# Optimization experiments

Measured on AMD Instinct MI355X. Metric: run time of the kernel, lower is better.

Reference implementation:

```python
import jax, jax.numpy as jnp
import numpy as np

D_MODEL = 1024
HEADS = 16
D_K = D_MODEL // HEADS
B, S = 2, 2048


def setup_inputs() -> dict:
    key = jax.random.key(0)
    ks = jax.random.split(key, 11)
    sc = 1.0 / np.sqrt(D_MODEL)
    return {
        "q": jax.random.normal(ks[0], (B, S, D_MODEL), jnp.float32),
        "k": jax.random.normal(ks[1], (B, S, D_MODEL), jnp.float32),
        "v": jax.random.normal(ks[2], (B, S, D_MODEL), jnp.float32),
        "Wq": jax.random.normal(ks[3], (D_MODEL, D_MODEL), jnp.float32) * sc,
        "bq": jnp.zeros((D_MODEL,), jnp.float32),
        "Wk": jax.random.normal(ks[4], (D_MODEL, D_MODEL), jnp.float32) * sc,
        "bk": jnp.zeros((D_MODEL,), jnp.float32),
        "Wv": jax.random.normal(ks[5], (D_MODEL, D_MODEL), jnp.float32) * sc,
        "bv": jnp.zeros((D_MODEL,), jnp.float32),
        "Wo": jax.random.normal(ks[6], (D_MODEL, D_MODEL), jnp.float32) * sc,
        "bo": jnp.zeros((D_MODEL,), jnp.float32),
    }


def reference(q, k, v, Wq, bq, Wk, bk, Wv, bv, Wo, bo):
    bs = q.shape[0]
    # linear projections then split heads: [B,S,D] -> [B,H,S,Dk]
    def proj(x, W, b):
        y = x @ W.T + b
        return y.reshape(bs, -1, HEADS, D_K).transpose(0, 2, 1, 3)

    qh = proj(q, Wq, bq)
    kh = proj(k, Wk, bk)
    vh = proj(v, Wv, bv)
    # scores: [B,H,Sq,Sk] -- full attention matrix as in the original
    scores = jnp.einsum("bhqd,bhkd->bhqk", qh, kh) / jnp.sqrt(
        jnp.asarray(D_K, jnp.float32))
    attn = jax.nn.softmax(scores, axis=-1)
    # dropout is identity in eval/reference mode
    out = jnp.einsum("bhqk,bhkd->bhqd", attn, vh)
    concat = out.transpose(0, 2, 1, 3).reshape(bs, -1, D_MODEL)
    return concat @ Wo.T + bo
```

## Files before the change

kernel.cpp:

```cpp
#include <hip/hip_runtime.h>
#include <hip/hip_bf16.h>

typedef __attribute__((ext_vector_type(8))) short bf16x8;
typedef __attribute__((ext_vector_type(4))) float f32x4;
typedef __attribute__((ext_vector_type(16))) float f32x16;

#define DM   1024
#define SEQ  2048
#define NB   2
#define NH   16
#define MR   (NB*SEQ)

#define SMK  (MR*DM)
#define W1M  (DM*DM)

#define QSCALE 0.18033688011112042f

#define OFF_QB  ((size_t)0)
#define OFF_KB  ((size_t)SMK)
#define OFF_VB  ((size_t)(2*(size_t)SMK))
#define OFF_WQ  ((size_t)(3*(size_t)SMK))
#define OFF_WO  ((size_t)(3*(size_t)SMK + 3*(size_t)W1M))
#define OFF_QP  ((size_t)(3*(size_t)SMK + 4*(size_t)W1M))
#define OFF_KP  ((size_t)(4*(size_t)SMK + 4*(size_t)W1M))
#define OFF_VP  ((size_t)(5*(size_t)SMK + 4*(size_t)W1M))
#define OFF_CC  ((size_t)0)

__device__ __forceinline__ unsigned short f2bf(float f) {
  union { __hip_bfloat16 b; unsigned short u; } cv;
  cv.b = __float2bfloat16(f);
  return cv.u;
}

__device__ __forceinline__ unsigned int cvtpk_bf16(float lo, float hi) {
  unsigned int r;
  asm("v_cvt_pk_bf16_f32 %0, %1, %2" : "=v"(r) : "v"(lo), "v"(hi));
  return r;
}

__device__ __forceinline__ void plane32_swap(unsigned int& a, unsigned int& b) {
  asm("v_permlane32_swap_b32 %0, %1" : "+v"(a), "+v"(b));
}

__global__ __launch_bounds__(256) void cvt_inputs(const float* __restrict__ q,
                                                  const float* __restrict__ k,
                                                  const float* __restrict__ v,
                                                  unsigned short* __restrict__ dst) {
  const int z = blockIdx.y;
  const float* src = (z == 0) ? q : ((z == 1) ? k : v);
  int i = blockIdx.x * 256 + threadIdx.x;
  float4 val = reinterpret_cast<const float4*>(src)[i];
  ushort4 o;
  o.x = f2bf(val.x); o.y = f2bf(val.y); o.z = f2bf(val.z); o.w = f2bf(val.w);
  reinterpret_cast<ushort4*>(dst + (size_t)z * SMK)[i] = o;
}

__global__ __launch_bounds__(256) void cvt_weights(const float* __restrict__ wq,
                                                   const float* __restrict__ wk,
                                                   const float* __restrict__ wv,
                                                   const float* __restrict__ wo,
                                                   unsigned short* __restrict__ dst) {
  const int z = blockIdx.y;
  const float* src = (z == 0) ? wq : ((z == 1) ? wk : ((z == 2) ? wv : wo));
  int i = blockIdx.x * 256 + threadIdx.x;
  float4 val = reinterpret_cast<const float4*>(src)[i];
  ushort4 o;
  o.x = f2bf(val.x); o.y = f2bf(val.y); o.z = f2bf(val.z); o.w = f2bf(val.w);
  reinterpret_cast<ushort4*>(dst + (size_t)z * W1M)[i] = o;
}

__device__ __forceinline__ void gload_lds16(const void* g, void* l) {
  __builtin_amdgcn_global_load_lds(
      (const __attribute__((address_space(1))) unsigned int*)g,
      (__attribute__((address_space(3))) unsigned int*)l,
      16, 0, 0);
}

template<int BM, int BN, bool OUT_BF16, bool BIAS_ROW>
__device__ __forceinline__ void gemm_bt_body(unsigned short* __restrict__ As,
                                             unsigned short* __restrict__ Bs,
                                             const unsigned short* __restrict__ A,
                                             const unsigned short* __restrict__ Bt,
                                             const float* __restrict__ bias,
                                             void* __restrict__ Cv,
                                             int N, int K, float scale,
                                             int brow, int bcol) {
  constexpr int MREP = BM / 32;
  constexpr int NREP = BN / 32;
  constexpr int LPS  = BM / 64 + BN / 64;
  const int tid  = threadIdx.x;
  const int lane = tid & 63;
  const int w    = tid >> 6;
  const int wr   = w >> 1, wc = w & 1;

  f32x4 acc[MREP][NREP];
#pragma unroll
  for (int m = 0; m < MREP; m++)
#pragma unroll
    for (int n = 0; n < NREP; n++) acc[m][n] = (f32x4){0.f, 0.f, 0.f, 0.f};

  const int srow = lane >> 2;
  const int scol = (lane & 3) * 8;

  auto stage = [&](int buf, int k0) {
#pragma unroll
    for (int c = w; c < BM / 16; c += 4)
      gload_lds16(A + (size_t)(brow + c * 16 + srow) * K + k0 + scol,
                  (char*)As + (size_t)buf * BM * 64 + c * 1024);
#pragma unroll
    for (int c = w; c < BN / 16; c += 4)
      gload_lds16(Bt + (size_t)(bcol + c * 16 + srow) * K + k0 + scol,
                  (char*)Bs + (size_t)buf * BN * 64 + c * 1024);
  };

  stage(0, 0);
  stage(1, 32);

  const int nk = K / 32;
  const int lrow_a = wr * (BM / 2) + (lane & 15);
  const int lrow_b = wc * (BN / 2) + (lane & 15);
  const int lcol   = (lane >> 4) * 8;

  int b0 = 0;
  for (int kt = 0; kt < nk; ++kt) {
    if (kt + 1 < nk) {
      if constexpr (LPS == 4) asm volatile("s_waitcnt vmcnt(4)" ::: "memory");
      else                    asm volatile("s_waitcnt vmcnt(3)" ::: "memory");
    } else {
      asm volatile("s_waitcnt vmcnt(0)" ::: "memory");
    }
    __builtin_amdgcn_s_barrier();
    __builtin_amdgcn_sched_barrier(0);
    if (kt + 2 < nk) {
      int bn = b0 + 2; if (bn >= 3) bn -= 3;
      stage(bn, (kt + 2) * 32);
    }
    bf16x8 a[MREP], b[NREP];
#pragma unroll
    for (int m = 0; m < MREP; m++)
      a[m] = *(const bf16x8*)&As[(size_t)b0 * BM * 32 + (lrow_a + m * 16) * 32 + lcol];
#pragma unroll
    for (int n = 0; n < NREP; n++)
      b[n] = *(const bf16x8*)&Bs[(size_t)b0 * BN * 32 + (lrow_b + n * 16) * 32 + lcol];
    __builtin_amdgcn_s_setprio(1);
#pragma unroll
    for (int m = 0; m < MREP; m++)
#pragma unroll
      for (int n = 0; n < NREP; n++)
        acc[m][n] = __builtin_amdgcn_mfma_f32_16x16x32_bf16(a[m], b[n], acc[m][n], 0, 0, 0);
    __builtin_amdgcn_s_setprio(0);
    b0 = (b0 == 2) ? 0 : b0 + 1;
  }

  const int crow0 = brow + wr * (BM / 2);
  const int ccol0 = bcol + wc * (BN / 2);
  const int rsub  = (lane >> 4) * 4;
  const int csub  = lane & 15;
#pragma unroll
  for (int m = 0; m < MREP; m++)
#pragma unroll
    for (int n = 0; n < NREP; n++) {
      int col = ccol0 + n * 16 + csub;
      float bcol_v = BIAS_ROW ? 0.f : bias[col];
#pragma unroll
      for (int qq = 0; qq < 4; qq++) {
        int row = crow0 + m * 16 + rsub + qq;
        float bb = BIAS_ROW ? bias[row] : bcol_v;
        float v = (acc[m][n][qq] + bb) * scale;
        if (OUT_BF16)
          ((unsigned short*)Cv)[(size_t)row * N + col] = f2bf(v);
        else
          ((float*)Cv)[(size_t)row * N + col] = v;
      }
    }
}

__global__ __launch_bounds__(256) void gemm_qkv(unsigned short* ws,
                                                const float* __restrict__ bq,
                                                const float* __restrict__ bk,
                                                const float* __restrict__ bv) {
  __shared__ unsigned short As[3 * 128 * 32];
  __shared__ unsigned short Bs[3 * 128 * 32];
  const int z = blockIdx.z;
  const int bid = blockIdx.x;
  if (z < 2) {
    int bx = bid & 7, by = bid >> 3;
    gemm_bt_body<128, 128, true, false>(
        As, Bs,
        ws + OFF_QB + (size_t)z * SMK, ws + OFF_WQ + (size_t)z * W1M,
        z ? bk : bq, ws + OFF_QP + (size_t)z * SMK,
        DM, DM, z ? 1.f : QSCALE, by * 128, bx * 128);
  } else {
    int bx = bid & 31, by = bid >> 5;
    gemm_bt_body<128, 128, true, true>(
        As, Bs,
        ws + OFF_WQ + 2 * W1M, ws + OFF_VB,
        bv, ws + OFF_VP,
        MR, DM, 1.f, by * 128, bx * 128);
  }
}

__global__ __launch_bounds__(256) void gemm_out(const unsigned short* __restrict__ ws,
                                                const float* __restrict__ bo,
                                                float* __restrict__ out) {
  __shared__ unsigned short As[3 * 64 * 32];
  __shared__ unsigned short Bs[3 * 128 * 32];
  gemm_bt_body<64, 128, false, false>(
      As, Bs,
      ws + OFF_CC, ws + OFF_WO, bo, out,
      DM, DM, 1.f, blockIdx.y * 64, blockIdx.x * 128);
}

__global__ __launch_bounds__(512, 2) void flash_attn(unsigned short* ws) {
  __shared__ __align__(16) unsigned char smem[98304];

  const int tid  = threadIdx.x;
  const int lane = tid & 63;
  const int w    = tid >> 6;
  const int s    = w >> 2;
  const int wsub = w & 3;
  const int q    = lane & 31;
  const int hi   = lane >> 5;
  const int swq  = q & 7;
  const int bid  = blockIdx.x;
  const int swzb = (bid & 7) * 32 + (bid >> 3);
  const int qblk = swzb & 7;
  const int bh   = swzb >> 3;
  const int b    = bh >> 4, h = bh & 15;

  const unsigned short* Qp = ws + OFF_QP;
  const unsigned short* Kp = ws + OFF_KP;
  const unsigned short* Vp = ws + OFF_VP;
  unsigned short* CC = ws + OFF_CC;

  const unsigned short* Kg = Kp + (size_t)(b * SEQ) * DM + h * 64;
  const unsigned short* Vg = Vp + (size_t)(h * 64) * MR + (size_t)b * SEQ;

  bf16x8 bqf[2][4];
#pragma unroll
  for (int s2 = 0; s2 < 2; s2++) {
    const unsigned short* qrow =
        Qp + (size_t)(b * SEQ + qblk * 256 + wsub * 64 + s2 * 32 + q) * DM + h * 64;
#pragma unroll
    for (int c = 0; c < 4; c++)
      bqf[s2][c] = *(const bf16x8*)(qrow + c * 16 + hi * 8);
  }

  f32x16 o_acc[2][2];
  float l_run[2] = {0.f, 0.f};
#pragma unroll
  for (int s2 = 0; s2 < 2; s2++)
#pragma unroll
    for (int dt = 0; dt < 2; dt++)
#pragma unroll
      for (int r = 0; r < 16; r++) o_acc[s2][dt][r] = 0.f;

  auto stage = [&](int buf, int t) {
    const unsigned short* Kt = Kg + (size_t)(s * 16 + t) * 64 * DM;
    const unsigned short* Vt = Vg + (s * 16 + t) * 64;
    char* base = (char*)smem + (size_t)(s * 3 + buf) * 16384;
#pragma unroll
    for (int i = 0; i < 2; i++) {
      int slot = wsub * 128 + i * 64 + lane;
      int srow = slot >> 3;
      int gch  = (slot & 7) ^ (srow & 7);
      gload_lds16(Kt + (size_t)srow * DM + gch * 8, base + slot * 16);
      gload_lds16(Vt + (size_t)srow * MR + gch * 8, base + 8192 + slot * 16);
    }
  };

  stage(0, 0);
  stage(1, 1);

  int bcur = 0;
  for (int t = 0; t < 16; ++t) {
    if (t < 15) asm volatile("s_waitcnt vmcnt(4)" ::: "memory");
    else        asm volatile("s_waitcnt vmcnt(0)" ::: "memory");
    __builtin_amdgcn_s_barrier();
    __builtin_amdgcn_sched_barrier(0);
    if (t + 2 < 16) {
      int bn = bcur + 2; if (bn >= 3) bn -= 3;
      stage(bn, t + 2);
    }
    const unsigned short* Kb = (const unsigned short*)(smem + (size_t)(s * 3 + bcur) * 16384);
    const unsigned short* Vb = Kb + 4096;

    f32x16 st[2][2];
#pragma unroll
    for (int s2 = 0; s2 < 2; s2++)
#pragma unroll
      for (int r = 0; r < 16; r++) { st[s2][0][r] = 0.f; st[s2][1][r] = 0.f; }
    __builtin_amdgcn_s_setprio(1);
#pragma unroll
    for (int c = 0; c < 4; c++) {
      int ch = (((c << 1) | hi) ^ swq) << 3;
      bf16x8 ak0 = *(const bf16x8*)&Kb[q * 64 + ch];
      bf16x8 ak1 = *(const bf16x8*)&Kb[(32 + q) * 64 + ch];
      st[0][0] = __builtin_amdgcn_mfma_f32_32x32x16_bf16(ak0, bqf[0][c], st[0][0], 0, 0, 0);
      st[0][1] = __builtin_amdgcn_mfma_f32_32x32x16_bf16(ak1, bqf[0][c], st[0][1], 0, 0, 0);
      st[1][0] = __builtin_amdgcn_mfma_f32_32x32x16_bf16(ak0, bqf[1][c], st[1][0], 0, 0, 0);
      st[1][1] = __builtin_amdgcn_mfma_f32_32x32x16_bf16(ak1, bqf[1][c], st[1][1], 0, 0, 0);
    }
    __builtin_amdgcn_s_setprio(0);

    unsigned int pk[2][2][8];
#pragma unroll
    for (int s2 = 0; s2 < 2; s2++) {
      float lt = 0.f;
#pragma unroll
      for (int p = 0; p < 8; p++) {
        float e0 = __builtin_amdgcn_exp2f(st[s2][0][2 * p]);
        float e1 = __builtin_amdgcn_exp2f(st[s2][0][2 * p + 1]);
        float e2 = __builtin_amdgcn_exp2f(st[s2][1][2 * p]);
        float e3 = __builtin_amdgcn_exp2f(st[s2][1][2 * p + 1]);
        lt += (e0 + e1) + (e2 + e3);
        pk[s2][0][p] = cvtpk_bf16(e0, e1);
        pk[s2][1][p] = cvtpk_bf16(e2, e3);
      }
      l_run[s2] += lt;
      plane32_swap(pk[s2][0][0], pk[s2][0][2]); plane32_swap(pk[s2][0][1], pk[s2][0][3]);
      plane32_swap(pk[s2][0][4], pk[s2][0][6]); plane32_swap(pk[s2][0][5], pk[s2][0][7]);
      plane32_swap(pk[s2][1][0], pk[s2][1][2]); plane32_swap(pk[s2][1][1], pk[s2][1][3]);
      plane32_swap(pk[s2][1][4], pk[s2][1][6]); plane32_swap(pk[s2][1][5], pk[s2][1][7]);
    }

    __builtin_amdgcn_s_setprio(1);
#pragma unroll
    for (int t4 = 0; t4 < 4; t4++) {
      int ch = (((t4 << 1) | hi) ^ swq) << 3;
      union { unsigned int u[4]; bf16x8 v; } pb0, pb1;
#pragma unroll
      for (int j = 0; j < 4; j++) {
        pb0.u[j] = pk[0][t4 >> 1][(t4 & 1) * 4 + j];
        pb1.u[j] = pk[1][t4 >> 1][(t4 & 1) * 4 + j];
      }
#pragma unroll
      for (int dt = 0; dt < 2; dt++) {
        bf16x8 av = *(const bf16x8*)&Vb[(dt * 32 + q) * 64 + ch];
        o_acc[0][dt] = __builtin_amdgcn_mfma_f32_32x32x16_bf16(av, pb0.v, o_acc[0][dt], 0, 0, 0);
        o_acc[1][dt] = __builtin_amdgcn_mfma_f32_32x32x16_bf16(av, pb1.v, o_acc[1][dt], 0, 0, 0);
      }
    }
    __builtin_amdgcn_s_setprio(0);
    bcur = (bcur == 2) ? 0 : bcur + 1;
  }

  __syncthreads();
  float* scr = (float*)smem;
  float lsum[2];
#pragma unroll
  for (int s2 = 0; s2 < 2; s2++)
    lsum[s2] = l_run[s2] + __shfl_xor(l_run[s2], 32, 64);
  const int gi = wsub * 64 + lane;
  if (s == 1) {
#pragma unroll
    for (int s2 = 0; s2 < 2; s2++) {
#pragma unroll
      for (int dt = 0; dt < 2; dt++)
#pragma unroll
        for (int r = 0; r < 16; r++)
          scr[gi * 67 + s2 * 33 + dt * 16 + r] = o_acc[s2][dt][r];
      scr[gi * 67 + s2 * 33 + 32] = lsum[s2];
    }
  }
  __syncthreads();
  if (s == 0) {
#pragma unroll
    for (int s2 = 0; s2 < 2; s2++) {
#pragma unroll
      for (int dt = 0; dt < 2; dt++)
#pragma unroll
        for (int r = 0; r < 16; r++)
          o_acc[s2][dt][r] += scr[gi * 67 + s2 * 33 + dt * 16 + r];
      float l = lsum[s2] + scr[gi * 67 + s2 * 33 + 32];
      float inv = 1.f / l;

      int qg = b * SEQ + qblk * 256 + wsub * 64 + s2 * 32 + q;
      unsigned short* crow = CC + (size_t)qg * DM + h * 64;
#pragma unroll
      for (int dt = 0; dt < 2; dt++)
#pragma unroll
        for (int rq = 0; rq < 4; rq++) {
          ushort4 o;
          o.x = f2bf(o_acc[s2][dt][4 * rq + 0] * inv);
          o.y = f2bf(o_acc[s2][dt][4 * rq + 1] * inv);
          o.z = f2bf(o_acc[s2][dt][4 * rq + 2] * inv);
          o.w = f2bf(o_acc[s2][dt][4 * rq + 3] * inv);
          *(ushort4*)&crow[dt * 32 + rq * 8 + hi * 4] = o;
        }
    }
  }
}

extern "C" void kernel_launch(void* const* d_in, const int* in_sizes, int n_in,
                              void* d_out, int out_size, void* d_ws, size_t ws_size,
                              hipStream_t stream) {
  const float* q  = (const float*)d_in[0];
  const float* k  = (const float*)d_in[1];
  const float* v  = (const float*)d_in[2];
  const float* Wq = (const float*)d_in[3];
  const float* bq = (const float*)d_in[4];
  const float* Wk = (const float*)d_in[5];
  const float* bk = (const float*)d_in[6];
  const float* Wv = (const float*)d_in[7];
  const float* bv = (const float*)d_in[8];
  const float* Wo = (const float*)d_in[9];
  const float* bo = (const float*)d_in[10];

  unsigned short* ws = (unsigned short*)d_ws;
  float* out = (float*)d_out;

  cvt_inputs<<<dim3(SMK / 1024, 3), dim3(256), 0, stream>>>(q, k, v, ws + OFF_QB);
  cvt_weights<<<dim3(W1M / 1024, 4), dim3(256), 0, stream>>>(Wq, Wk, Wv, Wo, ws + OFF_WQ);

  gemm_qkv<<<dim3(256, 1, 3), dim3(256), 0, stream>>>(ws, bq, bk, bv);

  flash_attn<<<dim3(256), dim3(512), 0, stream>>>(ws);

  gemm_out<<<dim3(DM / 128, MR / 64, 1), dim3(256), 0, stream>>>(ws, bo, out);
}
```

Before: 120.9 us.

## Split flash attention KV range across three blocks and combine in separate kernel

After: 215.8 us. 1.78x slower.

```diff
diff --git a/kernel.cpp b/kernel.cpp
--- a/kernel.cpp
+++ b/kernel.cpp
@@ -30,6 +30,12 @@
   union { __hip_bfloat16 b; unsigned short u; } cv;
   cv.b = __float2bfloat16(f);
   return cv.u;
+}
+
+__device__ __forceinline__ float bf2f(unsigned short u) {
+  union { unsigned int i; float f; } cv;
+  cv.i = (unsigned int)u << 16;
+  return cv.f;
 }
 
 __device__ __forceinline__ unsigned int cvtpk_bf16(float lo, float hi) {
@@ -211,27 +217,28 @@
       DM, DM, 1.f, blockIdx.y * 64, blockIdx.x * 128);
 }
 
-__global__ __launch_bounds__(512, 2) void flash_attn(unsigned short* ws) {
-  __shared__ __align__(16) unsigned char smem[98304];
+__global__ __launch_bounds__(256, 3) void flash_attn(unsigned short* ws) {
+  __shared__ __align__(16) unsigned char smem[49152];
 
   const int tid  = threadIdx.x;
   const int lane = tid & 63;
-  const int w    = tid >> 6;
-  const int s    = w >> 2;
-  const int wsub = w & 3;
+  const int wsub = tid >> 6;
   const int q    = lane & 31;
   const int hi   = lane >> 5;
   const int swq  = q & 7;
   const int bid  = blockIdx.x;
-  const int swzb = (bid & 7) * 32 + (bid >> 3);
-  const int qblk = swzb & 7;
-  const int bh   = swzb >> 3;
+  const int swzb = (bid & 7) * 96 + (bid >> 3);
+  const int bh   = swzb / 24;
+  const int r24  = swzb % 24;
+  const int qblk = r24 / 3;
+  const int s    = r24 % 3;
   const int b    = bh >> 4, h = bh & 15;
+  const int kt0  = s * 11;
+  const int nt   = (s == 2) ? 10 : 11;
 
   const unsigned short* Qp = ws + OFF_QP;
   const unsigned short* Kp = ws + OFF_KP;
   const unsigned short* Vp = ws + OFF_VP;
-  unsigned short* CC = ws + OFF_CC;
 
   const unsigned short* Kg = Kp + (size_t)(b * SEQ) * DM + h * 64;
   const unsigned short* Vg = Vp + (size_t)(h * 64) * MR + (size_t)b * SEQ;
@@ -246,19 +253,24 @@
       bqf[s2][c] = *(const bf16x8*)(qrow + c * 16 + hi * 8);
   }
 
+  const bf16x8 kOnes = {16256, 16256, 16256, 16256, 16256, 16256, 16256, 16256};
+
   f32x16 o_acc[2][2];
-  float l_run[2] = {0.f, 0.f};
-#pragma unroll
-  for (int s2 = 0; s2 < 2; s2++)
+  f32x16 o_l[2];
+#pragma unroll
+  for (int s2 = 0; s2 < 2; s2++) {
+#pragma unroll
+    for (int r = 0; r < 16; r++) o_l[s2][r] = 0.f;
 #pragma unroll
     for (int dt = 0; dt < 2; dt++)
 #pragma unroll
       for (int r = 0; r < 16; r++) o_acc[s2][dt][r] = 0.f;
-
-  auto stage = [&](int buf, int t) {
-    const unsigned short* Kt = Kg + (size_t)(s * 16 + t) * 64 * DM;
-    const unsigned short* Vt = Vg + (s * 16 + t) * 64;
-    char* base = (char*)smem + (size_t)(s * 3 + buf) * 16384;
+  }
+
+  auto stage = [&](int buf, int kt) {
+    const unsigned short* Kt = Kg + (size_t)kt * 64 * DM;
+    const unsigned short* Vt = Vg + kt * 64;
+    char* base = (char*)smem + (size_t)buf * 16384;
 #pragma unroll
     for (int i = 0; i < 2; i++) {
       int slot = wsub * 128 + i * 64 + lane;
@@ -269,20 +281,20 @@
     }
   };
 
-  stage(0, 0);
-  stage(1, 1);
+  stage(0, kt0);
+  stage(1, kt0 + 1);
 
   int bcur = 0;
-  for (int t = 0; t < 16; ++t) {
-    if (t < 15) asm volatile("s_waitcnt vmcnt(4)" ::: "memory");
-    else        asm volatile("s_waitcnt vmcnt(0)" ::: "memory");
+  for (int t = 0; t < nt; ++t) {
+    if (t < nt - 1) asm volatile("s_waitcnt vmcnt(4)" ::: "memory");
+    else            asm volatile("s_waitcnt vmcnt(0)" ::: "memory");
     __builtin_amdgcn_s_barrier();
     __builtin_amdgcn_sched_barrier(0);
-    if (t + 2 < 16) {
+    if (t + 2 < nt) {
       int bn = bcur + 2; if (bn >= 3) bn -= 3;
-      stage(bn, t + 2);
-    }
-    const unsigned short* Kb = (const unsigned short*)(smem + (size_t)(s * 3 + bcur) * 16384);
+      stage(bn, kt0 + t + 2);
+    }
+    const unsigned short* Kb = (const unsigned short*)(smem + (size_t)bcur * 16384);
     const unsigned short* Vb = Kb + 4096;
 
     f32x16 st[2][2];
@@ -306,18 +318,15 @@
     unsigned int pk[2][2][8];
 #pragma unroll
     for (int s2 = 0; s2 < 2; s2++) {
-      float lt = 0.f;
 #pragma unroll
       for (int p = 0; p < 8; p++) {
         float e0 = __builtin_amdgcn_exp2f(st[s2][0][2 * p]);
         float e1 = __builtin_amdgcn_exp2f(st[s2][0][2 * p + 1]);
         float e2 = __builtin_amdgcn_exp2f(st[s2][1][2 * p]);
         float e3 = __builtin_amdgcn_exp2f(st[s2][1][2 * p + 1]);
-        lt += (e0 + e1) + (e2 + e3);
         pk[s2][0][p] = cvtpk_bf16(e0, e1);
         pk[s2][1][p] = cvtpk_bf16(e2, e3);
       }
-      l_run[s2] += lt;
       plane32_swap(pk[s2][0][0], pk[s2][0][2]); plane32_swap(pk[s2][0][1], pk[s2][0][3]);
       plane32_swap(pk[s2][0][4], pk[s2][0][6]); plane32_swap(pk[s2][0][5], pk[s2][0][7]);
       plane32_swap(pk[s2][1][0], pk[s2][1][2]); plane32_swap(pk[s2][1][1], pk[s2][1][3]);
@@ -334,6 +343,8 @@
         pb0.u[j] = pk[0][t4 >> 1][(t4 & 1) * 4 + j];
         pb1.u[j] = pk[1][t4 >> 1][(t4 & 1) * 4 + j];
       }
+      o_l[0] = __builtin_amdgcn_mfma_f32_32x32x16_bf16(kOnes, pb0.v, o_l[0], 0, 0, 0);
+      o_l[1] = __builtin_amdgcn_mfma_f32_32x32x16_bf16(kOnes, pb1.v, o_l[1], 0, 0, 0);
 #pragma unroll
       for (int dt = 0; dt < 2; dt++) {
         bf16x8 av = *(const bf16x8*)&Vb[(dt * 32 + q) * 64 + ch];
@@ -345,51 +356,50 @@
     bcur = (bcur == 2) ? 0 : bcur + 1;
   }
 
-  __syncthreads();
-  float* scr = (float*)smem;
-  float lsum[2];
-#pragma unroll
-  for (int s2 = 0; s2 < 2; s2++)
-    lsum[s2] = l_run[s2] + __shfl_xor(l_run[s2], 32, 64);
-  const int gi = wsub * 64 + lane;
-  if (s == 1) {
-#pragma unroll
-    for (int s2 = 0; s2 < 2; s2++) {
-#pragma unroll
-      for (int dt = 0; dt < 2; dt++)
-#pragma unroll
-        for (int r = 0; r < 16; r++)
-          scr[gi * 67 + s2 * 33 + dt * 16 + r] = o_acc[s2][dt][r];
-      scr[gi * 67 + s2 * 33 + 32] = lsum[s2];
-    }
-  }
-  __syncthreads();
-  if (s == 0) {
-#pragma unroll
-    for (int s2 = 0; s2 < 2; s2++) {
-#pragma unroll
-      for (int dt = 0; dt < 2; dt++)
-#pragma unroll
-        for (int r = 0; r < 16; r++)
-          o_acc[s2][dt][r] += scr[gi * 67 + s2 * 33 + dt * 16 + r];
-      float l = lsum[s2] + scr[gi * 67 + s2 * 33 + 32];
-      float inv = 1.f / l;
-
-      int qg = b * SEQ + qblk * 256 + wsub * 64 + s2 * 32 + q;
-      unsigned short* crow = CC + (size_t)qg * DM + h * 64;
-#pragma unroll
-      for (int dt = 0; dt < 2; dt++)
-#pragma unroll
-        for (int rq = 0; rq < 4; rq++) {
-          ushort4 o;
-          o.x = f2bf(o_acc[s2][dt][4 * rq + 0] * inv);
-          o.y = f2bf(o_acc[s2][dt][4 * rq + 1] * inv);
-          o.z = f2bf(o_acc[s2][dt][4 * rq + 2] * inv);
-          o.w = f2bf(o_acc[s2][dt][4 * rq + 3] * inv);
-          *(ushort4*)&crow[dt * 32 + rq * 8 + hi * 4] = o;
-        }
-    }
-  }
+  unsigned short* Pp = ws + (size_t)s * SMK;
+  float* lf = (float*)(ws + OFF_WQ);
+#pragma unroll
+  for (int s2 = 0; s2 < 2; s2++) {
+    int srow = qblk * 256 + wsub * 64 + s2 * 32 + q;
+    lf[((s * NB + b) * NH + h) * SEQ + srow] = o_l[s2][0];
+    int qg = b * SEQ + srow;
+    unsigned short* prow = Pp + (size_t)qg * DM + h * 64;
+#pragma unroll
+    for (int dt = 0; dt < 2; dt++)
+#pragma unroll
+      for (int rq = 0; rq < 4; rq++) {
+        ushort4 o;
+        o.x = f2bf(o_acc[s2][dt][4 * rq + 0]);
+        o.y = f2bf(o_acc[s2][dt][4 * rq + 1]);
+        o.z = f2bf(o_acc[s2][dt][4 * rq + 2]);
+        o.w = f2bf(o_acc[s2][dt][4 * rq + 3]);
+        *(ushort4*)&prow[dt * 32 + rq * 8 + hi * 4] = o;
+      }
+  }
+}
+
+__global__ __launch_bounds__(256) void combine_splits(unsigned short* ws) {
+  int i = blockIdx.x * 256 + threadIdx.x;
+  size_t e0 = (size_t)i * 8;
+  int row = (int)(e0 >> 10);
+  int col = (int)(e0 & 1023);
+  int b = row >> 11, srow = row & 2047, h = col >> 6;
+  const float* lf = (const float*)(ws + OFF_WQ);
+  float l = lf[((0 * NB + b) * NH + h) * SEQ + srow]
+          + lf[((1 * NB + b) * NH + h) * SEQ + srow]
+          + lf[((2 * NB + b) * NH + h) * SEQ + srow];
+  float inv = 1.f / l;
+  bf16x8 p0 = *(const bf16x8*)(ws + OFF_QB + e0);
+  bf16x8 p1 = *(const bf16x8*)(ws + OFF_KB + e0);
+  bf16x8 p2 = *(const bf16x8*)(ws + OFF_VB + e0);
+  bf16x8 o;
+#pragma unroll
+  for (int j = 0; j < 8; j++) {
+    float f = (bf2f((unsigned short)p0[j]) + bf2f((unsigned short)p1[j])
+             + bf2f((unsigned short)p2[j])) * inv;
+    o[j] = (short)f2bf(f);
+  }
+  *(bf16x8*)(ws + OFF_CC + e0) = o;
 }
 
 extern "C" void kernel_launch(void* const* d_in, const int* in_sizes, int n_in,
@@ -415,7 +425,9 @@
 
   gemm_qkv<<<dim3(256, 1, 3), dim3(256), 0, stream>>>(ws, bq, bk, bv);
 
-  flash_attn<<<dim3(256), dim3(512), 0, stream>>>(ws);
+  flash_attn<<<dim3(768), dim3(256), 0, stream>>>(ws);
+
+  combine_splits<<<dim3(2048), dim3(256), 0, stream>>>(ws);
 
   gemm_out<<<dim3(DM / 128, MR / 64, 1), dim3(256), 0, stream>>>(ws, bo, out);
 }
```
